# Performance work log

Measured on AMD Instinct MI355X. Metric: run time of the kernel, lower is better.

Reference implementation:

```python
import jax, jax.numpy as jnp
import numpy as np

N_NODES = 50000
N_EDGES = 800000
D_FEAT = 64


def setup_inputs() -> dict:
    key = jax.random.key(0)
    k1, k2, k3, k4 = jax.random.split(key, 4)
    rows = jnp.sort(jax.random.randint(k1, (N_EDGES,), 0, N_NODES, dtype=jnp.int64))
    cols = jax.random.randint(k2, (N_EDGES,), 0, N_NODES, dtype=jnp.int64)
    vals = jax.random.uniform(k3, (N_EDGES,), dtype=jnp.float32)
    embeds = jax.random.normal(k4, (N_NODES, D_FEAT), dtype=jnp.float32)
    return {"rows": rows, "cols": cols, "vals": vals, "embeds": embeds}


def reference(rows, cols, vals, embeds):
    # torch.spmm(adj, embeds) with adj in COO form:
    # out[r] = sum_{e: rows[e]==r} vals[e] * embeds[cols[e]]
    gathered = vals[:, None] * embeds[cols]            # [E, D]
    out = jax.ops.segment_sum(gathered, rows, num_segments=N_NODES)  # [N, D]
    return out
```

## Files before the change

### kernel.cpp

```cpp
#include <hip/hip_runtime.h>
#include <hip/hip_fp16.h>


#define D_FEAT 64
#define BLOCK 256

__global__ __launch_bounds__(BLOCK) void build_row_ptr_edges(
    const int* __restrict__ rows, int* __restrict__ row_ptr,
    int n_nodes, int n_edges)
{
    const int e = blockIdx.x * BLOCK + threadIdx.x;
    if (e >= n_edges) return;
    const int r  = rows[e];
    const int rp = (e == 0) ? -1 : rows[e - 1];
    for (int v = rp + 1; v <= r; ++v) row_ptr[v] = e;
    if (e == n_edges - 1)
        for (int v = r + 1; v <= n_nodes; ++v) row_ptr[v] = n_edges;
}

__global__ __launch_bounds__(BLOCK) void cvt_f32_f16(
    const float* __restrict__ in, __half* __restrict__ out, int n4)
{
    const int i = blockIdx.x * BLOCK + threadIdx.x;
    if (i >= n4) return;
    const float4 x = ((const float4*)in)[i];
    __half2 a = __floats2half2_rn(x.x, x.y);
    __half2 b = __floats2half2_rn(x.z, x.w);
    ((__half2*)out)[2 * i]     = a;
    ((__half2*)out)[2 * i + 1] = b;
}

__global__ __launch_bounds__(BLOCK) void spmm_row_f16(
    const int* __restrict__ row_ptr,
    const int* __restrict__ cols,
    const float* __restrict__ vals,
    const __half* __restrict__ embeds_h,
    float* __restrict__ out,
    int n_nodes)
{
    const int wave = (int)((blockIdx.x * (unsigned)BLOCK + threadIdx.x) >> 6);
    if (wave >= n_nodes) return;
    const int lane = (int)(threadIdx.x & 63u);
    const int sub  = lane >> 4;
    const int f4   = lane & 15;

    const int s = row_ptr[wave];
    const int t = row_ptr[wave + 1];
    if (s >= t) {
        if (lane < 16)
            ((float4*)(out + (size_t)wave * D_FEAT))[f4] = make_float4(0.f,0.f,0.f,0.f);
        return;
    }

    float4 acc = make_float4(0.f, 0.f, 0.f, 0.f);

    for (int e = s; e < t; e += 16) {
        const int tm1 = t - 1;
        const int i0 = e + sub, i1 = i0 + 4, i2 = i0 + 8, i3 = i0 + 12;
        const int j0 = i0 < tm1 ? i0 : tm1;
        const int j1 = i1 < tm1 ? i1 : tm1;
        const int j2 = i2 < tm1 ? i2 : tm1;
        const int j3 = i3 < tm1 ? i3 : tm1;
        const int c0 = cols[j0], c1 = cols[j1], c2 = cols[j2], c3 = cols[j3];
        float v0 = vals[j0], v1 = vals[j1], v2 = vals[j2], v3 = vals[j3];
        if (i0 > tm1) v0 = 0.f;
        if (i1 > tm1) v1 = 0.f;
        if (i2 > tm1) v2 = 0.f;
        if (i3 > tm1) v3 = 0.f;
        const uint2 p0 = ((const uint2*)(embeds_h + (size_t)c0 * D_FEAT))[f4];
        const uint2 p1 = ((const uint2*)(embeds_h + (size_t)c1 * D_FEAT))[f4];
        const uint2 p2 = ((const uint2*)(embeds_h + (size_t)c2 * D_FEAT))[f4];
        const uint2 p3 = ((const uint2*)(embeds_h + (size_t)c3 * D_FEAT))[f4];

        {
            float2 a = __half22float2(*(const __half2*)&p0.x);
            float2 b = __half22float2(*(const __half2*)&p0.y);
            acc.x = fmaf(v0, a.x, acc.x); acc.y = fmaf(v0, a.y, acc.y);
            acc.z = fmaf(v0, b.x, acc.z); acc.w = fmaf(v0, b.y, acc.w);
        }
        {
            float2 a = __half22float2(*(const __half2*)&p1.x);
            float2 b = __half22float2(*(const __half2*)&p1.y);
            acc.x = fmaf(v1, a.x, acc.x); acc.y = fmaf(v1, a.y, acc.y);
            acc.z = fmaf(v1, b.x, acc.z); acc.w = fmaf(v1, b.y, acc.w);
        }
        {
            float2 a = __half22float2(*(const __half2*)&p2.x);
            float2 b = __half22float2(*(const __half2*)&p2.y);
            acc.x = fmaf(v2, a.x, acc.x); acc.y = fmaf(v2, a.y, acc.y);
            acc.z = fmaf(v2, b.x, acc.z); acc.w = fmaf(v2, b.y, acc.w);
        }
        {
            float2 a = __half22float2(*(const __half2*)&p3.x);
            float2 b = __half22float2(*(const __half2*)&p3.y);
            acc.x = fmaf(v3, a.x, acc.x); acc.y = fmaf(v3, a.y, acc.y);
            acc.z = fmaf(v3, b.x, acc.z); acc.w = fmaf(v3, b.y, acc.w);
        }
    }

    acc.x += __shfl_xor(acc.x, 16, 64);
    acc.y += __shfl_xor(acc.y, 16, 64);
    acc.z += __shfl_xor(acc.z, 16, 64);
    acc.w += __shfl_xor(acc.w, 16, 64);
    acc.x += __shfl_xor(acc.x, 32, 64);
    acc.y += __shfl_xor(acc.y, 32, 64);
    acc.z += __shfl_xor(acc.z, 32, 64);
    acc.w += __shfl_xor(acc.w, 32, 64);

    if (lane < 16)
        ((float4*)(out + (size_t)wave * D_FEAT))[f4] = acc;
}

extern "C" void kernel_launch(void* const* d_in, const int* in_sizes, int n_in,
                              void* d_out, int out_size, void* d_ws, size_t ws_size,
                              hipStream_t stream) {
    const int*   rows   = (const int*)d_in[0];
    const int*   cols   = (const int*)d_in[1];
    const float* vals   = (const float*)d_in[2];
    const float* embeds = (const float*)d_in[3];
    float*       out    = (float*)d_out;

    const int n_edges = in_sizes[0];
    const int n_nodes = out_size / D_FEAT;
    const int n_feat_total = n_nodes * D_FEAT;

    int*    row_ptr  = (int*)d_ws;
    __half* embeds_h = (__half*)((char*)d_ws + (1 << 18));

    {
        const int nblocks = (n_edges + BLOCK - 1) / BLOCK;
        build_row_ptr_edges<<<nblocks, BLOCK, 0, stream>>>(rows, row_ptr, n_nodes, n_edges);
    }
    {
        const int n4 = n_feat_total / 4;
        const int nblocks = (n4 + BLOCK - 1) / BLOCK;
        cvt_f32_f16<<<nblocks, BLOCK, 0, stream>>>(embeds, embeds_h, n4);
    }
    {
        const int waves_per_block = BLOCK / 64;
        const int nblocks = (n_nodes + waves_per_block - 1) / waves_per_block;
        spmm_row_f16<<<nblocks, BLOCK, 0, stream>>>(row_ptr, cols, vals, embeds_h, out, n_nodes);
    }
}
```

Baseline: 98.13 us.

## Fuse setup kernels and split SpMM into two column-range passes

Merges the row-pointer build and the fp16 conversion into one launch to save a kernel launch. Splits the SpMM into two passes that each gather only half of the column range, so each pass's working set of embeddings (about 3.2 MB fp16) fits better in cache; the second pass accumulates into the output. Output writes use nontemporal stores. The cost is reading cols and vals twice, one extra read-modify-write of the output, and wasted gather slots for masked edges.

```diff
diff --git a/kernel.cpp b/kernel.cpp
--- a/kernel.cpp
+++ b/kernel.cpp
@@ -5,38 +5,40 @@
 #define D_FEAT 64
 #define BLOCK 256
 
-__global__ __launch_bounds__(BLOCK) void build_row_ptr_edges(
+typedef float f32x4 __attribute__((ext_vector_type(4)));
+
+__global__ __launch_bounds__(BLOCK) void setup_fused(
     const int* __restrict__ rows, int* __restrict__ row_ptr,
-    int n_nodes, int n_edges)
+    const float* __restrict__ embeds, __half* __restrict__ embeds_h,
+    int n_nodes, int n_edges, int n4, int nb_rp)
 {
-    const int e = blockIdx.x * BLOCK + threadIdx.x;
-    if (e >= n_edges) return;
-    const int r  = rows[e];
-    const int rp = (e == 0) ? -1 : rows[e - 1];
-    for (int v = rp + 1; v <= r; ++v) row_ptr[v] = e;
-    if (e == n_edges - 1)
-        for (int v = r + 1; v <= n_nodes; ++v) row_ptr[v] = n_edges;
+    if ((int)blockIdx.x < nb_rp) {
+        const int e = blockIdx.x * BLOCK + threadIdx.x;
+        if (e >= n_edges) return;
+        const int r  = rows[e];
+        const int rp = (e == 0) ? -1 : rows[e - 1];
+        for (int v = rp + 1; v <= r; ++v) row_ptr[v] = e;
+        if (e == n_edges - 1)
+            for (int v = r + 1; v <= n_nodes; ++v) row_ptr[v] = n_edges;
+    } else {
+        const int i = ((int)blockIdx.x - nb_rp) * BLOCK + (int)threadIdx.x;
+        if (i >= n4) return;
+        const float4 x = ((const float4*)embeds)[i];
+        __half2 a = __floats2half2_rn(x.x, x.y);
+        __half2 b = __floats2half2_rn(x.z, x.w);
+        ((__half2*)embeds_h)[2 * i]     = a;
+        ((__half2*)embeds_h)[2 * i + 1] = b;
+    }
 }
 
-__global__ __launch_bounds__(BLOCK) void cvt_f32_f16(
-    const float* __restrict__ in, __half* __restrict__ out, int n4)
-{
-    const int i = blockIdx.x * BLOCK + threadIdx.x;
-    if (i >= n4) return;
-    const float4 x = ((const float4*)in)[i];
-    __half2 a = __floats2half2_rn(x.x, x.y);
-    __half2 b = __floats2half2_rn(x.z, x.w);
-    ((__half2*)out)[2 * i]     = a;
-    ((__half2*)out)[2 * i + 1] = b;
-}
-
-__global__ __launch_bounds__(BLOCK) void spmm_row_f16(
+template <int ACCUM>
+__global__ __launch_bounds__(BLOCK) void spmm_pass(
     const int* __restrict__ row_ptr,
     const int* __restrict__ cols,
     const float* __restrict__ vals,
     const __half* __restrict__ embeds_h,
     float* __restrict__ out,
-    int n_nodes)
+    int n_nodes, int lo, int hi)
 {
     const int wave = (int)((blockIdx.x * (unsigned)BLOCK + threadIdx.x) >> 6);
     if (wave >= n_nodes) return;
@@ -47,10 +49,15 @@
     const int s = row_ptr[wave];
     const int t = row_ptr[wave + 1];
     if (s >= t) {
-        if (lane < 16)
-            ((float4*)(out + (size_t)wave * D_FEAT))[f4] = make_float4(0.f,0.f,0.f,0.f);
+        if (!ACCUM && lane < 16) {
+            f32x4 z = (f32x4)(0.f);
+            __builtin_nontemporal_store(z, (f32x4*)(out + wave * D_FEAT) + f4);
+        }
         return;
     }
+
+    const char* eb = (const char*)embeds_h;
+    const int foff = f4 << 3;
 
     float4 acc = make_float4(0.f, 0.f, 0.f, 0.f);
 
@@ -61,16 +68,21 @@
         const int j1 = i1 < tm1 ? i1 : tm1;
         const int j2 = i2 < tm1 ? i2 : tm1;
         const int j3 = i3 < tm1 ? i3 : tm1;
-        const int c0 = cols[j0], c1 = cols[j1], c2 = cols[j2], c3 = cols[j3];
+        int c0 = cols[j0], c1 = cols[j1], c2 = cols[j2], c3 = cols[j3];
         float v0 = vals[j0], v1 = vals[j1], v2 = vals[j2], v3 = vals[j3];
-        if (i0 > tm1) v0 = 0.f;
-        if (i1 > tm1) v1 = 0.f;
-        if (i2 > tm1) v2 = 0.f;
-        if (i3 > tm1) v3 = 0.f;
-        const uint2 p0 = ((const uint2*)(embeds_h + (size_t)c0 * D_FEAT))[f4];
-        const uint2 p1 = ((const uint2*)(embeds_h + (size_t)c1 * D_FEAT))[f4];
-        const uint2 p2 = ((const uint2*)(embeds_h + (size_t)c2 * D_FEAT))[f4];
-        const uint2 p3 = ((const uint2*)(embeds_h + (size_t)c3 * D_FEAT))[f4];
+        const bool ok0 = (i0 <= tm1) & (c0 >= lo) & (c0 < hi);
+        const bool ok1 = (i1 <= tm1) & (c1 >= lo) & (c1 < hi);
+        const bool ok2 = (i2 <= tm1) & (c2 >= lo) & (c2 < hi);
+        const bool ok3 = (i3 <= tm1) & (c3 >= lo) & (c3 < hi);
+        v0 = ok0 ? v0 : 0.f;  c0 = ok0 ? c0 : lo;
+        v1 = ok1 ? v1 : 0.f;  c1 = ok1 ? c1 : lo;
+        v2 = ok2 ? v2 : 0.f;  c2 = ok2 ? c2 : lo;
+        v3 = ok3 ? v3 : 0.f;  c3 = ok3 ? c3 : lo;
+
+        const uint2 p0 = *(const uint2*)(eb + (((unsigned)c0 << 7) + foff));
+        const uint2 p1 = *(const uint2*)(eb + (((unsigned)c1 << 7) + foff));
+        const uint2 p2 = *(const uint2*)(eb + (((unsigned)c2 << 7) + foff));
+        const uint2 p3 = *(const uint2*)(eb + (((unsigned)c3 << 7) + foff));
 
         {
             float2 a = __half22float2(*(const __half2*)&p0.x);
@@ -107,8 +119,16 @@
     acc.z += __shfl_xor(acc.z, 32, 64);
     acc.w += __shfl_xor(acc.w, 32, 64);
 
-    if (lane < 16)
-        ((float4*)(out + (size_t)wave * D_FEAT))[f4] = acc;
+    if (lane < 16) {
+        f32x4* po = (f32x4*)(out + wave * D_FEAT) + f4;
+        f32x4 r;
+        r.x = acc.x; r.y = acc.y; r.z = acc.z; r.w = acc.w;
+        if (ACCUM) {
+            f32x4 old = __builtin_nontemporal_load(po);
+            r += old;
+        }
+        __builtin_nontemporal_store(r, po);
+    }
 }
 
 extern "C" void kernel_launch(void* const* d_in, const int* in_sizes, int n_in,
@@ -128,17 +148,19 @@
     __half* embeds_h = (__half*)((char*)d_ws + (1 << 18));
 
     {
-        const int nblocks = (n_edges + BLOCK - 1) / BLOCK;
-        build_row_ptr_edges<<<nblocks, BLOCK, 0, stream>>>(rows, row_ptr, n_nodes, n_edges);
+        const int n4 = n_feat_total / 4;
+        const int nb_rp  = (n_edges + BLOCK - 1) / BLOCK;
+        const int nb_cvt = (n4 + BLOCK - 1) / BLOCK;
+        setup_fused<<<nb_rp + nb_cvt, BLOCK, 0, stream>>>(
+            rows, row_ptr, embeds, embeds_h, n_nodes, n_edges, n4, nb_rp);
     }
     {
-        const int n4 = n_feat_total / 4;
-        const int nblocks = (n4 + BLOCK - 1) / BLOCK;
-        cvt_f32_f16<<<nblocks, BLOCK, 0, stream>>>(embeds, embeds_h, n4);
-    }
-    {
+        const int mid = n_nodes / 2;
         const int waves_per_block = BLOCK / 64;
         const int nblocks = (n_nodes + waves_per_block - 1) / waves_per_block;
-        spmm_row_f16<<<nblocks, BLOCK, 0, stream>>>(row_ptr, cols, vals, embeds_h, out, n_nodes);
+        spmm_pass<0><<<nblocks, BLOCK, 0, stream>>>(
+            row_ptr, cols, vals, embeds_h, out, n_nodes, 0, mid);
+        spmm_pass<1><<<nblocks, BLOCK, 0, stream>>>(
+            row_ptr, cols, vals, embeds_h, out, n_nodes, mid, n_nodes);
     }
 }
```

Result: slower. 120.3 us (+22.5%).
